# Kernel optimization log

Hardware: AMD Instinct MI355X
Metric: run time of the kernel (lower is better)

The kernel has to match this reference:

```python
import jax, jax.numpy as jnp
import numpy as np

TOP_K = 2
NUM_EXPERTS = 64
AUX_COEF = 0.01


def setup_inputs() -> dict:
    key = jax.random.key(0)
    kx, kw = jax.random.split(key)
    B, S, D, E = 4, 4096, 2048, NUM_EXPERTS
    x = jax.random.normal(kx, (B, S, D), dtype=jnp.float32)
    # nn.Linear default init ~ U(-1/sqrt(D), 1/sqrt(D))
    W = jax.random.uniform(kw, (E, D), dtype=jnp.float32,
                           minval=-1.0 / np.sqrt(D), maxval=1.0 / np.sqrt(D))
    return {"x": x, "W": W}


def reference(x, W):
    B, S, D = x.shape
    E = W.shape[0]
    # router projection (no bias)
    logits = jnp.einsum('bsd,ed->bse', x, W)          # [B,S,E]
    probs = jax.nn.softmax(logits, axis=-1)           # [B,S,E]
    top_k_gates, top_k_indices = jax.lax.top_k(probs, TOP_K)  # [B,S,K]
    top_k_gates = top_k_gates / (jnp.sum(top_k_gates, axis=-1, keepdims=True) + 1e-9)
    # aux loss: fraction of routed slots per expert (one-hot mean) x mean router prob
    total_slots = B * S * TOP_K
    counts = jnp.zeros((E,), dtype=jnp.float32).at[top_k_indices.reshape(-1)].add(1.0)
    avg_tokens_per_expert = counts / total_slots      # == one_hot(idx).mean(dims 0,1,2)
    avg_router_prob = jnp.mean(probs, axis=(0, 1))    # [E]
    aux_loss = AUX_COEF * E * jnp.sum(avg_tokens_per_expert * avg_router_prob)
    return top_k_indices, top_k_gates, aux_loss
```

## Files before the change

kernel.cpp:

```cpp
#include <hip/hip_runtime.h>
#include <math.h>

#define NTOK 16384
#define DDIM 2048
#define NEXP 64
#define TMB  64
#define NBLK (NTOK / TMB)
#define NCH  32
#define NS   64

typedef _Float16 half8v __attribute__((ext_vector_type(8)));
typedef float    f32x4  __attribute__((ext_vector_type(4)));

#define MFMA16(a, b, c) __builtin_amdgcn_mfma_f32_16x16x32_f16((a), (b), (c), 0, 0, 0)

__global__ __launch_bounds__(256) void prep_kernel(const float* __restrict__ W,
                                                   _Float16* __restrict__ Wh,
                                                   _Float16* __restrict__ Wl,
                                                   float* __restrict__ accg) {
    int idx = blockIdx.x * 256 + threadIdx.x;
    int e  = idx >> 8;
    int k0 = (idx & 255) << 3;
    const float* wp = W + (size_t)e * DDIM + k0;
    float4 w0 = *(const float4*)wp;
    float4 w1 = *(const float4*)(wp + 4);
    half8v h, l;
    h[0] = (_Float16)w0.x; l[0] = (_Float16)(w0.x - (float)h[0]);
    h[1] = (_Float16)w0.y; l[1] = (_Float16)(w0.y - (float)h[1]);
    h[2] = (_Float16)w0.z; l[2] = (_Float16)(w0.z - (float)h[2]);
    h[3] = (_Float16)w0.w; l[3] = (_Float16)(w0.w - (float)h[3]);
    h[4] = (_Float16)w1.x; l[4] = (_Float16)(w1.x - (float)h[4]);
    h[5] = (_Float16)w1.y; l[5] = (_Float16)(w1.y - (float)h[5]);
    h[6] = (_Float16)w1.z; l[6] = (_Float16)(w1.z - (float)h[6]);
    h[7] = (_Float16)w1.w; l[7] = (_Float16)(w1.w - (float)h[7]);
    int S = k0 >> 5, nb = e >> 4, nl = e & 15, q = (k0 >> 3) & 3;
    size_t off = (size_t)S * 2048 + nb * 512 + q * 128 + nl * 8;
    *(half8v*)&Wh[off] = h;
    *(half8v*)&Wl[off] = l;
    if (idx < 128) accg[idx] = 0.0f;
}

__device__ __forceinline__ void cvt8(float4 a, float4 b, half8v& h, half8v& l) {
    h[0]=(_Float16)a.x; l[0]=(_Float16)(a.x-(float)h[0]);
    h[1]=(_Float16)a.y; l[1]=(_Float16)(a.y-(float)h[1]);
    h[2]=(_Float16)a.z; l[2]=(_Float16)(a.z-(float)h[2]);
    h[3]=(_Float16)a.w; l[3]=(_Float16)(a.w-(float)h[3]);
    h[4]=(_Float16)b.x; l[4]=(_Float16)(b.x-(float)h[4]);
    h[5]=(_Float16)b.y; l[5]=(_Float16)(b.y-(float)h[5]);
    h[6]=(_Float16)b.z; l[6]=(_Float16)(b.z-(float)h[6]);
    h[7]=(_Float16)b.w; l[7]=(_Float16)(b.w-(float)h[7]);
}

__global__ __launch_bounds__(256, 1) void router_kernel(
    const float* __restrict__ x, const _Float16* __restrict__ Wh,
    const _Float16* __restrict__ Wl, float* __restrict__ accg,
    float* __restrict__ out)
{
    __shared__ __align__(16) _Float16 Ah[2][4096];
    __shared__ __align__(16) _Float16 Al[2][4096];
    __shared__ float lgt[TMB][NEXP + 1];
    __shared__ float cnt[NEXP];

    const int tid  = threadIdx.x;
    const int lane = tid & 63;
    const int wv   = __builtin_amdgcn_readfirstlane(tid >> 6);
    const int m0   = blockIdx.x * TMB;

    if (tid < NEXP) cnt[tid] = 0.0f;

    const int r    = tid >> 2;
    const int c0   = (tid & 3) * 16;
    const int tile = r >> 4, tok = r & 15;
    const int S0 = c0 >> 5,       q0 = (c0 >> 3) & 3;
    const int S1 = (c0+8) >> 5,   q1 = ((c0+8) >> 3) & 3;
    const int g0 = S0*64 + q0*16 + tok,  g1 = S1*64 + q1*16 + tok;
    const int off0 = tile*1024 + (g0 ^ ((g0>>4)&7)) * 8;
    const int off1 = tile*1024 + (g1 ^ ((g1>>4)&7)) * 8;

    const float* gx = x + (size_t)(m0 + r) * DDIM + c0;

    const int gr1 = 64 + lane;
    const int rd0 = (lane ^ ((lane>>4)&7)) * 8;
    const int rd1 = (gr1 ^ ((gr1>>4)&7)) * 8;

    const _Float16* whp = Wh + wv * 512 + lane * 8;
    const _Float16* wlp = Wl + wv * 512 + lane * 8;

    f32x4 acc0 = {0.f,0.f,0.f,0.f}, acc1 = {0.f,0.f,0.f,0.f};
    f32x4 acc2 = {0.f,0.f,0.f,0.f}, acc3 = {0.f,0.f,0.f,0.f};

    float4 xa0 = *(const float4*)(gx +  0), xa1 = *(const float4*)(gx +  4);
    float4 xa2 = *(const float4*)(gx +  8), xa3 = *(const float4*)(gx + 12);
    float4 xb0 = *(const float4*)(gx + 64), xb1 = *(const float4*)(gx + 68);
    float4 xb2 = *(const float4*)(gx + 72), xb3 = *(const float4*)(gx + 76);
    half8v wh0 = *(const half8v*)(whp);
    half8v wh1 = *(const half8v*)(whp + 2048);
    half8v wh2 = *(const half8v*)(whp + 4096);
    half8v wh3 = *(const half8v*)(whp + 6144);
    half8v wl0 = *(const half8v*)(wlp);
    half8v wl1 = *(const half8v*)(wlp + 2048);
    half8v wl2 = *(const half8v*)(wlp + 4096);
    half8v wl3 = *(const half8v*)(wlp + 6144);

#define CHUNK(ch, X0, X1, X2, X3, P, WHA, WLA, WHB, WLB)                    \
    {                                                                        \
        half8v h_, l_;                                                       \
        cvt8(X0, X1, h_, l_);                                                \
        *(half8v*)&Ah[P][off0] = h_;  *(half8v*)&Al[P][off0] = l_;           \
        cvt8(X2, X3, h_, l_);                                                \
        *(half8v*)&Ah[P][off1] = h_;  *(half8v*)&Al[P][off1] = l_;           \
        const int cf = ((ch) + 2 < NCH) ? (ch) + 2 : 0;                      \
        X0 = *(const float4*)(gx + cf * 64 +  0);                            \
        X1 = *(const float4*)(gx + cf * 64 +  4);                            \
        X2 = *(const float4*)(gx + cf * 64 +  8);                            \
        X3 = *(const float4*)(gx + cf * 64 + 12);                            \
        asm volatile("s_waitcnt lgkmcnt(0)" ::: "memory");                   \
        __builtin_amdgcn_s_barrier();                                        \
        {                                                \
            half8v a0h = *(const half8v*)&Ah[P][   0 + rd0];                 \
            half8v a0l = *(const half8v*)&Al[P][   0 + rd0];                 \
            half8v a1h = *(const half8v*)&Ah[P][1024 + rd0];                 \
            half8v a1l = *(const half8v*)&Al[P][1024 + rd0];                 \
            half8v a2h = *(const half8v*)&Ah[P][2048 + rd0];                 \
            half8v a2l = *(const half8v*)&Al[P][2048 + rd0];                 \
            half8v a3h = *(const half8v*)&Ah[P][3072 + rd0];                 \
            half8v a3l = *(const half8v*)&Al[P][3072 + rd0];                 \
            half8v bh = WHA, bl = WLA;                                       \
            const int SgN = (2 * (ch) + 4) & (NS - 1);                       \
            WHA = *(const half8v*)(whp + (size_t)SgN * 2048);                \
            WLA = *(const half8v*)(wlp + (size_t)SgN * 2048);                \
            acc0 = MFMA16(a0l, bh, acc0);                                    \
            acc0 = MFMA16(a0h, bl, acc0);                                    \
            acc0 = MFMA16(a0h, bh, acc0);                                    \
            acc1 = MFMA16(a1l, bh, acc1);                                    \
            acc1 = MFMA16(a1h, bl, acc1);                                    \
            acc1 = MFMA16(a1h, bh, acc1);                                    \
            acc2 = MFMA16(a2l, bh, acc2);                                    \
            acc2 = MFMA16(a2h, bl, acc2);                                    \
            acc2 = MFMA16(a2h, bh, acc2);                                    \
            acc3 = MFMA16(a3l, bh, acc3);                                    \
            acc3 = MFMA16(a3h, bl, acc3);                                    \
            acc3 = MFMA16(a3h, bh, acc3);                                    \
        }                                                                    \
        {                                              \
            half8v a0h = *(const half8v*)&Ah[P][   0 + rd1];                 \
            half8v a0l = *(const half8v*)&Al[P][   0 + rd1];                 \
            half8v a1h = *(const half8v*)&Ah[P][1024 + rd1];                 \
            half8v a1l = *(const half8v*)&Al[P][1024 + rd1];                 \
            half8v a2h = *(const half8v*)&Ah[P][2048 + rd1];                 \
            half8v a2l = *(const half8v*)&Al[P][2048 + rd1];                 \
            half8v a3h = *(const half8v*)&Ah[P][3072 + rd1];                 \
            half8v a3l = *(const half8v*)&Al[P][3072 + rd1];                 \
            half8v bh = WHB, bl = WLB;                                       \
            const int SgN = (2 * (ch) + 5) & (NS - 1);                       \
            WHB = *(const half8v*)(whp + (size_t)SgN * 2048);                \
            WLB = *(const half8v*)(wlp + (size_t)SgN * 2048);                \
            acc0 = MFMA16(a0l, bh, acc0);                                    \
            acc0 = MFMA16(a0h, bl, acc0);                                    \
            acc0 = MFMA16(a0h, bh, acc0);                                    \
            acc1 = MFMA16(a1l, bh, acc1);                                    \
            acc1 = MFMA16(a1h, bl, acc1);                                    \
            acc1 = MFMA16(a1h, bh, acc1);                                    \
            acc2 = MFMA16(a2l, bh, acc2);                                    \
            acc2 = MFMA16(a2h, bl, acc2);                                    \
            acc2 = MFMA16(a2h, bh, acc2);                                    \
            acc3 = MFMA16(a3l, bh, acc3);                                    \
            acc3 = MFMA16(a3h, bl, acc3);                                    \
            acc3 = MFMA16(a3h, bh, acc3);                                    \
        }                                                                    \
        \
        asm volatile("s_waitcnt lgkmcnt(0)" ::: "memory");                   \
        __builtin_amdgcn_s_barrier();                                        \
    }

    for (int cb = 0; cb < NCH; cb += 2) {
        CHUNK(cb + 0, xa0, xa1, xa2, xa3, 0, wh0, wl0, wh1, wl1);
        CHUNK(cb + 1, xb0, xb1, xb2, xb3, 1, wh2, wl2, wh3, wl3);
    }
#undef CHUNK

    {
        const int qr = lane >> 4;
        const int nl = lane & 15;
        #pragma unroll
        for (int rr = 0; rr < 4; ++rr) {
            const int mm = qr * 4 + rr;
            lgt[ 0 + mm][wv * 16 + nl] = acc0[rr];
            lgt[16 + mm][wv * 16 + nl] = acc1[rr];
            lgt[32 + mm][wv * 16 + nl] = acc2[rr];
            lgt[48 + mm][wv * 16 + nl] = acc3[rr];
        }
    }
    __syncthreads();

    for (int pass = 0; pass < 2; ++pass) {
        const int m = pass * 32 + (tid >> 3);
        const int j = tid & 7;
        float l[8];
        #pragma unroll
        for (int i = 0; i < 8; ++i) l[i] = lgt[m][j * 8 + i];

        float mx = l[0];
        #pragma unroll
        for (int i = 1; i < 8; ++i) mx = fmaxf(mx, l[i]);
        #pragma unroll
        for (int off = 1; off < 8; off <<= 1) mx = fmaxf(mx, __shfl_xor(mx, off, 8));

        float ev[8];
        float zs = 0.f;
        float v1 = -INFINITY, v2 = -INFINITY;
        int i1 = 0, i2 = 0;
        #pragma unroll
        for (int i = 0; i < 8; ++i) {
            ev[i] = __expf(l[i] - mx);
            zs += ev[i];
            int e = j * 8 + i;
            if (l[i] > v1)      { v2 = v1; i2 = i1; v1 = l[i]; i1 = e; }
            else if (l[i] > v2) { v2 = l[i]; i2 = e; }
        }
        #pragma unroll
        for (int off = 1; off < 8; off <<= 1) zs += __shfl_xor(zs, off, 8);

        #pragma unroll
        for (int off = 1; off < 8; off <<= 1) {
            float ov1 = __shfl_xor(v1, off, 8);
            int   oi1 = __shfl_xor(i1, off, 8);
            float ov2 = __shfl_xor(v2, off, 8);
            int   oi2 = __shfl_xor(i2, off, 8);
            bool afirst = (v1 > ov1) || (v1 == ov1 && i1 < oi1);
            if (afirst) {
                bool t = (v2 > ov1) || (v2 == ov1 && i2 < oi1);
                v2 = t ? v2 : ov1;
                i2 = t ? i2 : oi1;
            } else {
                bool t = (ov2 > v1) || (ov2 == v1 && oi2 < i1);
                v2 = t ? ov2 : v1;
                i2 = t ? oi2 : i1;
                v1 = ov1;
                i1 = oi1;
            }
        }

        const float invz = 1.0f / zs;
        if (j == 0) {
            float p1 = invz;
            float p2 = __expf(v2 - mx) * invz;
            float sden = p1 + p2 + 1e-9f;
            int tokg = m0 + m;
            out[tokg * 2 + 0] = (float)i1;
            out[tokg * 2 + 1] = (float)i2;
            out[32768 + tokg * 2 + 0] = p1 / sden;
            out[32768 + tokg * 2 + 1] = p2 / sden;
            atomicAdd(&cnt[i1], 1.0f);
            atomicAdd(&cnt[i2], 1.0f);
        }

        #pragma unroll
        for (int i = 0; i < 8; ++i) lgt[m][j * 8 + i] = ev[i] * invz;
    }
    __syncthreads();

    if (tid < NEXP) {
        atomicAdd(&accg[tid], cnt[tid]);
    } else if (tid < 128) {
        int e = tid - 64;
        float s = 0.f;
        #pragma unroll
        for (int t = 0; t < TMB; ++t) s += lgt[t][e];
        atomicAdd(&accg[64 + e], s);
    }
}

__global__ void finalize_kernel(const float* __restrict__ accg,
                                float* __restrict__ out)
{
    int t = threadIdx.x;
    float c = accg[t];
    float p = accg[64 + t];
    float term = (c / (float)(NTOK * 2)) * (p / (float)NTOK);
    #pragma unroll
    for (int off = 1; off < 64; off <<= 1) term += __shfl_xor(term, off, 64);
    if (t == 0) out[65536] = 0.01f * (float)NEXP * term;
}

extern "C" void kernel_launch(void* const* d_in, const int* in_sizes, int n_in,
                              void* d_out, int out_size, void* d_ws, size_t ws_size,
                              hipStream_t stream) {
    const float* x = (const float*)d_in[0];
    const float* W = (const float*)d_in[1];
    float* out  = (float*)d_out;
    float* accg = (float*)d_ws;
    _Float16* Wh = (_Float16*)(accg + 128);
    _Float16* Wl = Wh + (size_t)DDIM * NEXP;

    prep_kernel<<<64, 256, 0, stream>>>(W, Wh, Wl, accg);
    router_kernel<<<NBLK, 256, 0, stream>>>(x, Wh, Wl, accg, out);
    finalize_kernel<<<1, 64, 0, stream>>>(accg, out);
}
```

Measured before the change: 207.2 us.

## Split the K dimension across two wave groups with 512-thread blocks

The router block grows from 256 to 512 threads. Two groups of four waves each handle half of the 2048-wide reduction, using separate shared-memory staging buffers and half as many chunk iterations. Partial accumulators from the second group go through shared memory and are added before the softmax/top-k epilogue, which now runs in one pass over all 512 threads. This aims to raise wave count and memory-level parallelism per CU on a kernel bound by streaming x, at the cost of more shared memory and an extra reduction step.

Result: slower. 213.4 us (+3.0%).

```diff
diff --git a/kernel.cpp b/kernel.cpp
--- a/kernel.cpp
+++ b/kernel.cpp
@@ -6,8 +6,8 @@
 #define NEXP 64
 #define TMB  64
 #define NBLK (NTOK / TMB)
-#define NCH  32
-#define NS   64
+#define NCHH 16
+#define NSH  32
 
 typedef _Float16 half8v __attribute__((ext_vector_type(8)));
 typedef float    f32x4  __attribute__((ext_vector_type(4)));
@@ -51,40 +51,44 @@
     h[7]=(_Float16)b.w; l[7]=(_Float16)(b.w-(float)h[7]);
 }
 
-__global__ __launch_bounds__(256, 1) void router_kernel(
+__global__ __launch_bounds__(512, 1) void router_kernel(
     const float* __restrict__ x, const _Float16* __restrict__ Wh,
     const _Float16* __restrict__ Wl, float* __restrict__ accg,
     float* __restrict__ out)
 {
-    __shared__ __align__(16) _Float16 Ah[2][4096];
-    __shared__ __align__(16) _Float16 Al[2][4096];
+    __shared__ __align__(16) _Float16 Ah[2][2][4096];
+    __shared__ __align__(16) _Float16 Al[2][2][4096];
     __shared__ float lgt[TMB][NEXP + 1];
+    __shared__ float pacc[4][64][16];
     __shared__ float cnt[NEXP];
 
     const int tid  = threadIdx.x;
     const int lane = tid & 63;
     const int wv   = __builtin_amdgcn_readfirstlane(tid >> 6);
+    const int eb   = wv & 3;
+    const int kh   = wv >> 2;
     const int m0   = blockIdx.x * TMB;
 
     if (tid < NEXP) cnt[tid] = 0.0f;
 
-    const int r    = tid >> 2;
-    const int c0   = (tid & 3) * 16;
+    const int st   = tid & 255;
+    const int r    = st >> 2;
+    const int c0l  = (st & 3) * 16;
     const int tile = r >> 4, tok = r & 15;
-    const int S0 = c0 >> 5,       q0 = (c0 >> 3) & 3;
-    const int S1 = (c0+8) >> 5,   q1 = ((c0+8) >> 3) & 3;
+    const int S0 = c0l >> 5,       q0 = (c0l >> 3) & 3;
+    const int S1 = (c0l+8) >> 5,   q1 = ((c0l+8) >> 3) & 3;
     const int g0 = S0*64 + q0*16 + tok,  g1 = S1*64 + q1*16 + tok;
     const int off0 = tile*1024 + (g0 ^ ((g0>>4)&7)) * 8;
     const int off1 = tile*1024 + (g1 ^ ((g1>>4)&7)) * 8;
 
-    const float* gx = x + (size_t)(m0 + r) * DDIM + c0;
+    const float* gx = x + (size_t)(m0 + r) * DDIM + kh * 1024 + c0l;
 
     const int gr1 = 64 + lane;
     const int rd0 = (lane ^ ((lane>>4)&7)) * 8;
     const int rd1 = (gr1 ^ ((gr1>>4)&7)) * 8;
 
-    const _Float16* whp = Wh + wv * 512 + lane * 8;
-    const _Float16* wlp = Wl + wv * 512 + lane * 8;
+    const _Float16* whp = Wh + (size_t)kh * 65536 + eb * 512 + lane * 8;
+    const _Float16* wlp = Wl + (size_t)kh * 65536 + eb * 512 + lane * 8;
 
     f32x4 acc0 = {0.f,0.f,0.f,0.f}, acc1 = {0.f,0.f,0.f,0.f};
     f32x4 acc2 = {0.f,0.f,0.f,0.f}, acc3 = {0.f,0.f,0.f,0.f};
@@ -106,27 +110,27 @@
     {                                                                        \
         half8v h_, l_;                                                       \
         cvt8(X0, X1, h_, l_);                                                \
-        *(half8v*)&Ah[P][off0] = h_;  *(half8v*)&Al[P][off0] = l_;           \
+        *(half8v*)&Ah[kh][P][off0] = h_;  *(half8v*)&Al[kh][P][off0] = l_;   \
         cvt8(X2, X3, h_, l_);                                                \
-        *(half8v*)&Ah[P][off1] = h_;  *(half8v*)&Al[P][off1] = l_;           \
-        const int cf = ((ch) + 2 < NCH) ? (ch) + 2 : 0;                      \
+        *(half8v*)&Ah[kh][P][off1] = h_;  *(half8v*)&Al[kh][P][off1] = l_;   \
+        const int cf = ((ch) + 2 < NCHH) ? (ch) + 2 : 0;                     \
         X0 = *(const float4*)(gx + cf * 64 +  0);                            \
         X1 = *(const float4*)(gx + cf * 64 +  4);                            \
         X2 = *(const float4*)(gx + cf * 64 +  8);                            \
         X3 = *(const float4*)(gx + cf * 64 + 12);                            \
         asm volatile("s_waitcnt lgkmcnt(0)" ::: "memory");                   \
         __builtin_amdgcn_s_barrier();                                        \
-        {                                                \
-            half8v a0h = *(const half8v*)&Ah[P][   0 + rd0];                 \
-            half8v a0l = *(const half8v*)&Al[P][   0 + rd0];                 \
-            half8v a1h = *(const half8v*)&Ah[P][1024 + rd0];                 \
-            half8v a1l = *(const half8v*)&Al[P][1024 + rd0];                 \
-            half8v a2h = *(const half8v*)&Ah[P][2048 + rd0];                 \
-            half8v a2l = *(const half8v*)&Al[P][2048 + rd0];                 \
-            half8v a3h = *(const half8v*)&Ah[P][3072 + rd0];                 \
-            half8v a3l = *(const half8v*)&Al[P][3072 + rd0];                 \
+        {                                                     \
+            half8v a0h = *(const half8v*)&Ah[kh][P][   0 + rd0];             \
+            half8v a0l = *(const half8v*)&Al[kh][P][   0 + rd0];             \
+            half8v a1h = *(const half8v*)&Ah[kh][P][1024 + rd0];             \
+            half8v a1l = *(const half8v*)&Al[kh][P][1024 + rd0];             \
+            half8v a2h = *(const half8v*)&Ah[kh][P][2048 + rd0];             \
+            half8v a2l = *(const half8v*)&Al[kh][P][2048 + rd0];             \
+            half8v a3h = *(const half8v*)&Ah[kh][P][3072 + rd0];             \
+            half8v a3l = *(const half8v*)&Al[kh][P][3072 + rd0];             \
             half8v bh = WHA, bl = WLA;                                       \
-            const int SgN = (2 * (ch) + 4) & (NS - 1);                       \
+            const int SgN = (2 * (ch) + 4) & (NSH - 1);                      \
             WHA = *(const half8v*)(whp + (size_t)SgN * 2048);                \
             WLA = *(const half8v*)(wlp + (size_t)SgN * 2048);                \
             acc0 = MFMA16(a0l, bh, acc0);                                    \
@@ -142,17 +146,17 @@
             acc3 = MFMA16(a3h, bl, acc3);                                    \
             acc3 = MFMA16(a3h, bh, acc3);                                    \
         }                                                                    \
-        {                                              \
-            half8v a0h = *(const half8v*)&Ah[P][   0 + rd1];                 \
-            half8v a0l = *(const half8v*)&Al[P][   0 + rd1];                 \
-            half8v a1h = *(const half8v*)&Ah[P][1024 + rd1];                 \
-            half8v a1l = *(const half8v*)&Al[P][1024 + rd1];                 \
-            half8v a2h = *(const half8v*)&Ah[P][2048 + rd1];                 \
-            half8v a2l = *(const half8v*)&Al[P][2048 + rd1];                 \
-            half8v a3h = *(const half8v*)&Ah[P][3072 + rd1];                 \
-            half8v a3l = *(const half8v*)&Al[P][3072 + rd1];                 \
+        {                                                   \
+            half8v a0h = *(const half8v*)&Ah[kh][P][   0 + rd1];             \
+            half8v a0l = *(const half8v*)&Al[kh][P][   0 + rd1];             \
+            half8v a1h = *(const half8v*)&Ah[kh][P][1024 + rd1];             \
+            half8v a1l = *(const half8v*)&Al[kh][P][1024 + rd1];             \
+            half8v a2h = *(const half8v*)&Ah[kh][P][2048 + rd1];             \
+            half8v a2l = *(const half8v*)&Al[kh][P][2048 + rd1];             \
+            half8v a3h = *(const half8v*)&Ah[kh][P][3072 + rd1];             \
+            half8v a3l = *(const half8v*)&Al[kh][P][3072 + rd1];             \
             half8v bh = WHB, bl = WLB;                                       \
-            const int SgN = (2 * (ch) + 5) & (NS - 1);                       \
+            const int SgN = (2 * (ch) + 5) & (NSH - 1);                      \
             WHB = *(const half8v*)(whp + (size_t)SgN * 2048);                \
             WLB = *(const half8v*)(wlp + (size_t)SgN * 2048);                \
             acc0 = MFMA16(a0l, bh, acc0);                                    \
@@ -168,33 +172,43 @@
             acc3 = MFMA16(a3h, bl, acc3);                                    \
             acc3 = MFMA16(a3h, bh, acc3);                                    \
         }                                                                    \
-        \
         asm volatile("s_waitcnt lgkmcnt(0)" ::: "memory");                   \
         __builtin_amdgcn_s_barrier();                                        \
     }
 
-    for (int cb = 0; cb < NCH; cb += 2) {
+    for (int cb = 0; cb < NCHH; cb += 2) {
         CHUNK(cb + 0, xa0, xa1, xa2, xa3, 0, wh0, wl0, wh1, wl1);
         CHUNK(cb + 1, xb0, xb1, xb2, xb3, 1, wh2, wl2, wh3, wl3);
     }
 #undef CHUNK
 
-    {
+    if (kh == 1) {
+        #pragma unroll
+        for (int rr = 0; rr < 4; ++rr) {
+            pacc[eb][lane][ 0 + rr] = acc0[rr];
+            pacc[eb][lane][ 4 + rr] = acc1[rr];
+            pacc[eb][lane][ 8 + rr] = acc2[rr];
+            pacc[eb][lane][12 + rr] = acc3[rr];
+        }
+    }
+    __syncthreads();
+
+    if (kh == 0) {
         const int qr = lane >> 4;
         const int nl = lane & 15;
         #pragma unroll
         for (int rr = 0; rr < 4; ++rr) {
             const int mm = qr * 4 + rr;
-            lgt[ 0 + mm][wv * 16 + nl] = acc0[rr];
-            lgt[16 + mm][wv * 16 + nl] = acc1[rr];
-            lgt[32 + mm][wv * 16 + nl] = acc2[rr];
-            lgt[48 + mm][wv * 16 + nl] = acc3[rr];
+            lgt[ 0 + mm][eb * 16 + nl] = acc0[rr] + pacc[eb][lane][ 0 + rr];
+            lgt[16 + mm][eb * 16 + nl] = acc1[rr] + pacc[eb][lane][ 4 + rr];
+            lgt[32 + mm][eb * 16 + nl] = acc2[rr] + pacc[eb][lane][ 8 + rr];
+            lgt[48 + mm][eb * 16 + nl] = acc3[rr] + pacc[eb][lane][12 + rr];
         }
     }
     __syncthreads();
 
-    for (int pass = 0; pass < 2; ++pass) {
-        const int m = pass * 32 + (tid >> 3);
+    {
+        const int m = tid >> 3;
         const int j = tid & 7;
         float l[8];
         #pragma unroll
@@ -294,6 +308,6 @@
     _Float16* Wl = Wh + (size_t)DDIM * NEXP;
 
     prep_kernel<<<64, 256, 0, stream>>>(W, Wh, Wl, accg);
-    router_kernel<<<NBLK, 256, 0, stream>>>(x, Wh, Wl, accg, out);
+    router_kernel<<<NBLK, 512, 0, stream>>>(x, Wh, Wl, accg, out);
     finalize_kernel<<<1, 64, 0, stream>>>(accg, out);
 }
```

## Fuse weight split and finalize into router kernel, drop prep and finalize launches

Applied to the files above, without the earlier changes.

Removes the separate prep kernel that split W into fp16 high/low halves. The router kernel now loads fp32 W directly and converts it in registers on every step. The finalize kernel is also folded in: the last block, found with an atomic counter, computes the aux loss, and a memset zeroes the accumulators. This saves two kernel launches and their serialization, at the cost of redundant per-block W conversion and twice the W bytes read from cache.

Measured after the change: 208.0 us. No clear change (+0.4%).

```diff
diff --git a/kernel.cpp b/kernel.cpp
--- a/kernel.cpp
+++ b/kernel.cpp
@@ -13,32 +13,6 @@
 typedef float    f32x4  __attribute__((ext_vector_type(4)));
 
 #define MFMA16(a, b, c) __builtin_amdgcn_mfma_f32_16x16x32_f16((a), (b), (c), 0, 0, 0)
-
-__global__ __launch_bounds__(256) void prep_kernel(const float* __restrict__ W,
-                                                   _Float16* __restrict__ Wh,
-                                                   _Float16* __restrict__ Wl,
-                                                   float* __restrict__ accg) {
-    int idx = blockIdx.x * 256 + threadIdx.x;
-    int e  = idx >> 8;
-    int k0 = (idx & 255) << 3;
-    const float* wp = W + (size_t)e * DDIM + k0;
-    float4 w0 = *(const float4*)wp;
-    float4 w1 = *(const float4*)(wp + 4);
-    half8v h, l;
-    h[0] = (_Float16)w0.x; l[0] = (_Float16)(w0.x - (float)h[0]);
-    h[1] = (_Float16)w0.y; l[1] = (_Float16)(w0.y - (float)h[1]);
-    h[2] = (_Float16)w0.z; l[2] = (_Float16)(w0.z - (float)h[2]);
-    h[3] = (_Float16)w0.w; l[3] = (_Float16)(w0.w - (float)h[3]);
-    h[4] = (_Float16)w1.x; l[4] = (_Float16)(w1.x - (float)h[4]);
-    h[5] = (_Float16)w1.y; l[5] = (_Float16)(w1.y - (float)h[5]);
-    h[6] = (_Float16)w1.z; l[6] = (_Float16)(w1.z - (float)h[6]);
-    h[7] = (_Float16)w1.w; l[7] = (_Float16)(w1.w - (float)h[7]);
-    int S = k0 >> 5, nb = e >> 4, nl = e & 15, q = (k0 >> 3) & 3;
-    size_t off = (size_t)S * 2048 + nb * 512 + q * 128 + nl * 8;
-    *(half8v*)&Wh[off] = h;
-    *(half8v*)&Wl[off] = l;
-    if (idx < 128) accg[idx] = 0.0f;
-}
 
 __device__ __forceinline__ void cvt8(float4 a, float4 b, half8v& h, half8v& l) {
     h[0]=(_Float16)a.x; l[0]=(_Float16)(a.x-(float)h[0]);
@@ -52,14 +26,14 @@
 }
 
 __global__ __launch_bounds__(256, 1) void router_kernel(
-    const float* __restrict__ x, const _Float16* __restrict__ Wh,
-    const _Float16* __restrict__ Wl, float* __restrict__ accg,
-    float* __restrict__ out)
+    const float* __restrict__ x, const float* __restrict__ W,
+    float* __restrict__ accg, float* __restrict__ out)
 {
     __shared__ __align__(16) _Float16 Ah[2][4096];
     __shared__ __align__(16) _Float16 Al[2][4096];
     __shared__ float lgt[TMB][NEXP + 1];
     __shared__ float cnt[NEXP];
+    __shared__ int lastBlk;
 
     const int tid  = threadIdx.x;
     const int lane = tid & 63;
@@ -83,8 +57,7 @@
     const int rd0 = (lane ^ ((lane>>4)&7)) * 8;
     const int rd1 = (gr1 ^ ((gr1>>4)&7)) * 8;
 
-    const _Float16* whp = Wh + wv * 512 + lane * 8;
-    const _Float16* wlp = Wl + wv * 512 + lane * 8;
+    const float* wfp = W + (size_t)(wv * 16 + (lane & 15)) * DDIM + (lane >> 4) * 8;
 
     f32x4 acc0 = {0.f,0.f,0.f,0.f}, acc1 = {0.f,0.f,0.f,0.f};
     f32x4 acc2 = {0.f,0.f,0.f,0.f}, acc3 = {0.f,0.f,0.f,0.f};
@@ -93,22 +66,43 @@
     float4 xa2 = *(const float4*)(gx +  8), xa3 = *(const float4*)(gx + 12);
     float4 xb0 = *(const float4*)(gx + 64), xb1 = *(const float4*)(gx + 68);
     float4 xb2 = *(const float4*)(gx + 72), xb3 = *(const float4*)(gx + 76);
-    half8v wh0 = *(const half8v*)(whp);
-    half8v wh1 = *(const half8v*)(whp + 2048);
-    half8v wh2 = *(const half8v*)(whp + 4096);
-    half8v wh3 = *(const half8v*)(whp + 6144);
-    half8v wl0 = *(const half8v*)(wlp);
-    half8v wl1 = *(const half8v*)(wlp + 2048);
-    half8v wl2 = *(const half8v*)(wlp + 4096);
-    half8v wl3 = *(const half8v*)(wlp + 6144);
-
-#define CHUNK(ch, X0, X1, X2, X3, P, WHA, WLA, WHB, WLB)                    \
+    float4 w0a = *(const float4*)(wfp +  0), w0b = *(const float4*)(wfp +  4);
+    float4 w1a = *(const float4*)(wfp + 32), w1b = *(const float4*)(wfp + 36);
+    float4 w2a = *(const float4*)(wfp + 64), w2b = *(const float4*)(wfp + 68);
+    float4 w3a = *(const float4*)(wfp + 96), w3b = *(const float4*)(wfp + 100);
+
+#define STEPBODY(RD, BH, BL)                                                 \
     {                                                                        \
+        half8v a0h = *(const half8v*)&Ah[PB_][   0 + RD];                    \
+        half8v a0l = *(const half8v*)&Al[PB_][   0 + RD];                    \
+        half8v a1h = *(const half8v*)&Ah[PB_][1024 + RD];                    \
+        half8v a1l = *(const half8v*)&Al[PB_][1024 + RD];                    \
+        half8v a2h = *(const half8v*)&Ah[PB_][2048 + RD];                    \
+        half8v a2l = *(const half8v*)&Al[PB_][2048 + RD];                    \
+        half8v a3h = *(const half8v*)&Ah[PB_][3072 + RD];                    \
+        half8v a3l = *(const half8v*)&Al[PB_][3072 + RD];                    \
+        acc0 = MFMA16(a0l, BH, acc0);                                        \
+        acc0 = MFMA16(a0h, BL, acc0);                                        \
+        acc0 = MFMA16(a0h, BH, acc0);                                        \
+        acc1 = MFMA16(a1l, BH, acc1);                                        \
+        acc1 = MFMA16(a1h, BL, acc1);                                        \
+        acc1 = MFMA16(a1h, BH, acc1);                                        \
+        acc2 = MFMA16(a2l, BH, acc2);                                        \
+        acc2 = MFMA16(a2h, BL, acc2);                                        \
+        acc2 = MFMA16(a2h, BH, acc2);                                        \
+        acc3 = MFMA16(a3l, BH, acc3);                                        \
+        acc3 = MFMA16(a3h, BL, acc3);                                        \
+        acc3 = MFMA16(a3h, BH, acc3);                                        \
+    }
+
+#define CHUNK(ch, X0, X1, X2, X3, PB, WAa, WAb, WBa, WBb)                   \
+    {                                                                        \
+        const int PB_ = (PB);                                                \
         half8v h_, l_;                                                       \
         cvt8(X0, X1, h_, l_);                                                \
-        *(half8v*)&Ah[P][off0] = h_;  *(half8v*)&Al[P][off0] = l_;           \
+        *(half8v*)&Ah[PB_][off0] = h_;  *(half8v*)&Al[PB_][off0] = l_;       \
         cvt8(X2, X3, h_, l_);                                                \
-        *(half8v*)&Ah[P][off1] = h_;  *(half8v*)&Al[P][off1] = l_;           \
+        *(half8v*)&Ah[PB_][off1] = h_;  *(half8v*)&Al[PB_][off1] = l_;       \
         const int cf = ((ch) + 2 < NCH) ? (ch) + 2 : 0;                      \
         X0 = *(const float4*)(gx + cf * 64 +  0);                            \
         X1 = *(const float4*)(gx + cf * 64 +  4);                            \
@@ -117,67 +111,31 @@
         asm volatile("s_waitcnt lgkmcnt(0)" ::: "memory");                   \
         __builtin_amdgcn_s_barrier();                                        \
         {                                                \
-            half8v a0h = *(const half8v*)&Ah[P][   0 + rd0];                 \
-            half8v a0l = *(const half8v*)&Al[P][   0 + rd0];                 \
-            half8v a1h = *(const half8v*)&Ah[P][1024 + rd0];                 \
-            half8v a1l = *(const half8v*)&Al[P][1024 + rd0];                 \
-            half8v a2h = *(const half8v*)&Ah[P][2048 + rd0];                 \
-            half8v a2l = *(const half8v*)&Al[P][2048 + rd0];                 \
-            half8v a3h = *(const half8v*)&Ah[P][3072 + rd0];                 \
-            half8v a3l = *(const half8v*)&Al[P][3072 + rd0];                 \
-            half8v bh = WHA, bl = WLA;                                       \
+            half8v bh, bl;                                                   \
+            cvt8(WAa, WAb, bh, bl);                                          \
             const int SgN = (2 * (ch) + 4) & (NS - 1);                       \
-            WHA = *(const half8v*)(whp + (size_t)SgN * 2048);                \
-            WLA = *(const half8v*)(wlp + (size_t)SgN * 2048);                \
-            acc0 = MFMA16(a0l, bh, acc0);                                    \
-            acc0 = MFMA16(a0h, bl, acc0);                                    \
-            acc0 = MFMA16(a0h, bh, acc0);                                    \
-            acc1 = MFMA16(a1l, bh, acc1);                                    \
-            acc1 = MFMA16(a1h, bl, acc1);                                    \
-            acc1 = MFMA16(a1h, bh, acc1);                                    \
-            acc2 = MFMA16(a2l, bh, acc2);                                    \
-            acc2 = MFMA16(a2h, bl, acc2);                                    \
-            acc2 = MFMA16(a2h, bh, acc2);                                    \
-            acc3 = MFMA16(a3l, bh, acc3);                                    \
-            acc3 = MFMA16(a3h, bl, acc3);                                    \
-            acc3 = MFMA16(a3h, bh, acc3);                                    \
+            WAa = *(const float4*)(wfp + SgN * 32);                          \
+            WAb = *(const float4*)(wfp + SgN * 32 + 4);                      \
+            STEPBODY(rd0, bh, bl)                                            \
         }                                                                    \
         {                                              \
-            half8v a0h = *(const half8v*)&Ah[P][   0 + rd1];                 \
-            half8v a0l = *(const half8v*)&Al[P][   0 + rd1];                 \
-            half8v a1h = *(const half8v*)&Ah[P][1024 + rd1];                 \
-            half8v a1l = *(const half8v*)&Al[P][1024 + rd1];                 \
-            half8v a2h = *(const half8v*)&Ah[P][2048 + rd1];                 \
-            half8v a2l = *(const half8v*)&Al[P][2048 + rd1];                 \
-            half8v a3h = *(const half8v*)&Ah[P][3072 + rd1];                 \
-            half8v a3l = *(const half8v*)&Al[P][3072 + rd1];                 \
-            half8v bh = WHB, bl = WLB;                                       \
+            half8v bh, bl;                                                   \
+            cvt8(WBa, WBb, bh, bl);                                          \
             const int SgN = (2 * (ch) + 5) & (NS - 1);                       \
-            WHB = *(const half8v*)(whp + (size_t)SgN * 2048);                \
-            WLB = *(const half8v*)(wlp + (size_t)SgN * 2048);                \
-            acc0 = MFMA16(a0l, bh, acc0);                                    \
-            acc0 = MFMA16(a0h, bl, acc0);                                    \
-            acc0 = MFMA16(a0h, bh, acc0);                                    \
-            acc1 = MFMA16(a1l, bh, acc1);                                    \
-            acc1 = MFMA16(a1h, bl, acc1);                                    \
-            acc1 = MFMA16(a1h, bh, acc1);                                    \
-            acc2 = MFMA16(a2l, bh, acc2);                                    \
-            acc2 = MFMA16(a2h, bl, acc2);                                    \
-            acc2 = MFMA16(a2h, bh, acc2);                                    \
-            acc3 = MFMA16(a3l, bh, acc3);                                    \
-            acc3 = MFMA16(a3h, bl, acc3);                                    \
-            acc3 = MFMA16(a3h, bh, acc3);                                    \
+            WBa = *(const float4*)(wfp + SgN * 32);                          \
+            WBb = *(const float4*)(wfp + SgN * 32 + 4);                      \
+            STEPBODY(rd1, bh, bl)                                            \
         }                                                                    \
-        \
         asm volatile("s_waitcnt lgkmcnt(0)" ::: "memory");                   \
         __builtin_amdgcn_s_barrier();                                        \
     }
 
     for (int cb = 0; cb < NCH; cb += 2) {
-        CHUNK(cb + 0, xa0, xa1, xa2, xa3, 0, wh0, wl0, wh1, wl1);
-        CHUNK(cb + 1, xb0, xb1, xb2, xb3, 1, wh2, wl2, wh3, wl3);
+        CHUNK(cb + 0, xa0, xa1, xa2, xa3, 0, w0a, w0b, w1a, w1b);
+        CHUNK(cb + 1, xb0, xb1, xb2, xb3, 1, w2a, w2b, w3a, w3b);
     }
 #undef CHUNK
+#undef STEPBODY
 
     {
         const int qr = lane >> 4;
@@ -269,18 +227,24 @@
         for (int t = 0; t < TMB; ++t) s += lgt[t][e];
         atomicAdd(&accg[64 + e], s);
     }
-}
-
-__global__ void finalize_kernel(const float* __restrict__ accg,
-                                float* __restrict__ out)
-{
-    int t = threadIdx.x;
-    float c = accg[t];
-    float p = accg[64 + t];
-    float term = (c / (float)(NTOK * 2)) * (p / (float)NTOK);
-    #pragma unroll
-    for (int off = 1; off < 64; off <<= 1) term += __shfl_xor(term, off, 64);
-    if (t == 0) out[65536] = 0.01f * (float)NEXP * term;
+    __syncthreads();
+
+    if (tid == 0) {
+        __threadfence();
+        unsigned int old = atomicAdd((unsigned int*)(accg + 128), 1u);
+        lastBlk = (old == NBLK - 1) ? 1 : 0;
+    }
+    __syncthreads();
+    if (lastBlk && tid < 64) {
+        __threadfence();
+        const volatile float* ag = accg;
+        float c = ag[tid];
+        float p = ag[64 + tid];
+        float term = (c / (float)(NTOK * 2)) * (p / (float)NTOK);
+        #pragma unroll
+        for (int off = 1; off < 64; off <<= 1) term += __shfl_xor(term, off, 64);
+        if (tid == 0) out[65536] = 0.01f * (float)NEXP * term;
+    }
 }
 
 extern "C" void kernel_launch(void* const* d_in, const int* in_sizes, int n_in,
@@ -290,10 +254,7 @@
     const float* W = (const float*)d_in[1];
     float* out  = (float*)d_out;
     float* accg = (float*)d_ws;
-    _Float16* Wh = (_Float16*)(accg + 128);
-    _Float16* Wl = Wh + (size_t)DDIM * NEXP;
-
-    prep_kernel<<<64, 256, 0, stream>>>(W, Wh, Wl, accg);
-    router_kernel<<<NBLK, 256, 0, stream>>>(x, Wh, Wl, accg, out);
-    finalize_kernel<<<1, 64, 0, stream>>>(accg, out);
+
+    hipMemsetAsync(accg, 0, 1024, stream);
+    router_kernel<<<NBLK, 256, 0, stream>>>(x, W, accg, out);
 }
```
